# Optimization experiments

Hardware: AMD Instinct MI355X
Metric: run time of the kernel (lower is better)

## Reference

```python
import jax, jax.numpy as jnp
import numpy as np

HIDDEN = 4096
N_HEADS = 32
N_KV_HEADS = 8
HEAD_DIM = 128
ROPE_THETA = 1e6
RMS_EPS = 1e-6
SEQ = 2048


def setup_inputs() -> dict:
    key = jax.random.key(0)
    k1, k2, k3 = jax.random.split(key, 3)
    hidden_states = jax.random.normal(k1, (SEQ, HIDDEN), dtype=jnp.float32)
    # fused QKV weight: [hidden, (H + 2*Hkv) * head_dim]
    qkv_out = (N_HEADS + 2 * N_KV_HEADS) * HEAD_DIM
    w_qkv = jax.random.normal(k2, (HIDDEN, qkv_out), dtype=jnp.float32) * (HIDDEN ** -0.5)
    w_o = jax.random.normal(k3, (N_HEADS * HEAD_DIM, HIDDEN), dtype=jnp.float32) * ((N_HEADS * HEAD_DIM) ** -0.5)
    q_norm_w = jnp.ones((HEAD_DIM,), dtype=jnp.float32)
    k_norm_w = jnp.ones((HEAD_DIM,), dtype=jnp.float32)
    # NeoX-style rotary tables [T, head_dim/2]
    pos = jnp.arange(SEQ, dtype=jnp.float32)
    inv_freq = 1.0 / (ROPE_THETA ** (jnp.arange(0, HEAD_DIM, 2, dtype=jnp.float32) / HEAD_DIM))
    freqs = pos[:, None] * inv_freq[None, :]  # [T, d/2]
    cos = jnp.cos(freqs)
    sin = jnp.sin(freqs)
    return {"hidden_states": hidden_states, "cos": cos, "sin": sin,
            "w_qkv": w_qkv, "w_o": w_o, "q_norm_w": q_norm_w, "k_norm_w": k_norm_w}


def _rms_norm(x, w, eps=RMS_EPS):
    # per-head RMSNorm over last dim (head_dim)
    var = jnp.mean(jnp.square(x), axis=-1, keepdims=True)
    return x * jax.lax.rsqrt(var + eps) * w


def _rope(x, cos, sin):
    # NeoX rotate-half: x split into two halves of head_dim
    d2 = x.shape[-1] // 2
    x1, x2 = x[..., :d2], x[..., d2:]
    c = cos[:, None, :]  # [T,1,d/2] broadcast over heads
    s = sin[:, None, :]
    return jnp.concatenate([x1 * c - x2 * s, x2 * c + x1 * s], axis=-1)


def reference(hidden_states, cos, sin, w_qkv, w_o, q_norm_w, k_norm_w):
    T = hidden_states.shape[0]
    H, Hkv, D = N_HEADS, N_KV_HEADS, HEAD_DIM
    G = H // Hkv  # GQA group size
    scale = D ** -0.5

    qkv = hidden_states @ w_qkv  # [T, (H+2Hkv)*D]
    q, k, v = jnp.split(qkv, [H * D, (H + Hkv) * D], axis=1)
    q = q.reshape(T, H, D)
    k = k.reshape(T, Hkv, D)
    v = v.reshape(T, Hkv, D)

    q = _rms_norm(q, q_norm_w)
    k = _rms_norm(k, k_norm_w)
    q = _rope(q, cos, sin)
    k = _rope(k, cos, sin)

    # GQA: group query heads onto shared KV heads
    qg = q.reshape(T, Hkv, G, D)
    scores = jnp.einsum('qhgd,khd->hgqk', qg, k) * scale  # [Hkv,G,T,T]
    causal = jnp.tril(jnp.ones((T, T), dtype=bool))
    scores = jnp.where(causal, scores, jnp.float32(-1e30))
    probs = jax.nn.softmax(scores, axis=-1)
    out = jnp.einsum('hgqk,khd->qhgd', probs, v).reshape(T, H * D)
    return out @ w_o  # [T, hidden]
```

## Files before the change

### kernel.cpp

```cpp
#include <hip/hip_runtime.h>
#include <stdint.h>

#define SEQ   2048
#define HID   4096
#define NQH   32
#define NKVH  8
#define HD    128
#define QKVN  6144

typedef uint16_t u16;
typedef __attribute__((ext_vector_type(8))) short bf16x8;
typedef __attribute__((ext_vector_type(4))) float f32x4;
typedef __attribute__((ext_vector_type(4))) unsigned int u32x4;

static __device__ __forceinline__ float bf2f(u16 h){
  union { float f; unsigned int u; } v; v.u = ((unsigned int)h) << 16; return v.f;
}
static __device__ __forceinline__ u16 f2bf(float f){
  unsigned int u = __float_as_uint(f);
  return (u16)((u + 0x7fffu + ((u >> 16) & 1u)) >> 16);
}
static __device__ __forceinline__ f32x4 mfma16(bf16x8 a, bf16x8 b, f32x4 c){
  return __builtin_amdgcn_mfma_f32_16x16x32_bf16(a, b, c, 0, 0, 0);
}
static __device__ __forceinline__ void gload16(const void* g, void* l){
  __builtin_amdgcn_global_load_lds((const __attribute__((address_space(1))) void*)g,
                                   (__attribute__((address_space(3))) void*)l, 16, 0, 0);
}

__global__ void k_cvt(const float* __restrict__ src, u16* __restrict__ dst, int n4){
  int i = blockIdx.x * blockDim.x + threadIdx.x;
  if (i >= n4) return;
  float4 v = ((const float4*)src)[i];
  uint2 o;
  o.x = (unsigned)f2bf(v.x) | ((unsigned)f2bf(v.y) << 16);
  o.y = (unsigned)f2bf(v.z) | ((unsigned)f2bf(v.w) << 16);
  ((uint2*)dst)[i] = o;
}

__global__ void k_addf(const float* __restrict__ a, float* __restrict__ o, int n4){
  int i = blockIdx.x * blockDim.x + threadIdx.x;
  if (i >= n4) return;
  float4 x = ((const float4*)o)[i];
  float4 y = ((const float4*)a)[i];
  x.x += y.x; x.y += y.y; x.z += y.z; x.w += y.w;
  ((float4*)o)[i] = x;
}

__global__ void k_transpose_cvt(const float* __restrict__ src, u16* __restrict__ dst, int K, int N){
  __shared__ float t[32][33];
  int n0 = blockIdx.x * 32, k0 = blockIdx.y * 32;
  int tx = threadIdx.x, ty = threadIdx.y;
#pragma unroll
  for (int i = 0; i < 32; i += 8)
    t[ty + i][tx] = src[(size_t)(k0 + ty + i) * N + n0 + tx];
  __syncthreads();
#pragma unroll
  for (int i = 0; i < 32; i += 8)
    dst[(size_t)(n0 + ty + i) * K + k0 + tx] = f2bf(t[tx][ty + i]);
}

template<int OUTBF, int SPLITK, int XBC, int NBY>
__global__ __launch_bounds__(512) void k_gemm(const u16* __restrict__ A, const u16* __restrict__ Bt,
                                              void* __restrict__ Cv0, void* __restrict__ Cv1,
                                              int M, int N, int K){
  __shared__ __align__(16) u16 Asm[2][256][64];
  __shared__ __align__(16) u16 Bsm[2][256][64];
  const int tid = threadIdx.x, lane = tid & 63, wid = tid >> 6;
  const int wm = wid >> 2, wn = wid & 3;
  const int l16 = lane & 15, lhi = lane >> 4;
  const int rx = l16 & 7;
  const int bid = blockIdx.x;
  const int xcd = bid & 7, j = bid >> 3;
  const int bcol_i = xcd * XBC + j % XBC;
  const int rest = j / XBC;
  const int brow_i = rest % NBY;
  const int kz = (SPLITK > 1) ? (rest / NBY) : 0;
  const size_t brow = (size_t)brow_i * 256, bcol = (size_t)bcol_i * 256;
  const int kbeg = kz * (K / SPLITK);
  void* Cv = (kz == 0) ? Cv0 : Cv1;

  const f32x4 vz = {0.f, 0.f, 0.f, 0.f};
  f32x4 acc[8][4];
#pragma unroll
  for (int m = 0; m < 8; m++)
#pragma unroll
    for (int n = 0; n < 4; n++) acc[m][n] = vz;

  const int srow = lane >> 3;
  const int sg   = (lane & 7) ^ srow;
  const u16* Ags = A  + (brow + wid*8 + srow) * (size_t)K + sg*8 + kbeg;
  const u16* Bgs = Bt + (bcol + wid*8 + srow) * (size_t)K + sg*8 + kbeg;
  const int NT = (K / SPLITK) >> 6;

#pragma unroll
  for (int j2 = 0; j2 < 4; j2++) gload16(Ags + (size_t)j2*64*K, &Asm[0][wid*8 + j2*64][0]);
#pragma unroll
  for (int j2 = 0; j2 < 4; j2++) gload16(Bgs + (size_t)j2*64*K, &Bsm[0][wid*8 + j2*64][0]);
  asm volatile("s_waitcnt vmcnt(0)" ::: "memory");
  __builtin_amdgcn_sched_barrier(0);
  __builtin_amdgcn_s_barrier();

  for (int t = 0; t < NT; ++t){
    const int cur = t & 1, nxt = cur ^ 1;
    const size_t ko = (size_t)(t + 1) * 64;
    const bool st = (t + 1 < NT);
    bf16x8 a[8], b0, b1, b2, b3;
#pragma unroll
    for (int mi = 0; mi < 8; ++mi)
      a[mi] = *(const bf16x8*)&Asm[cur][wm*128 + mi*16 + l16][(lhi ^ rx) << 3];
    b0 = *(const bf16x8*)&Bsm[cur][wn*64 +  0 + l16][(lhi ^ rx) << 3];
    b1 = *(const bf16x8*)&Bsm[cur][wn*64 + 16 + l16][(lhi ^ rx) << 3];
    if (st){
      gload16(Ags + ko,                  &Asm[nxt][wid*8      ][0]);
      gload16(Ags + (size_t)64*K + ko,   &Asm[nxt][wid*8 +  64][0]);
      gload16(Bgs + ko,                  &Bsm[nxt][wid*8      ][0]);
      gload16(Bgs + (size_t)64*K + ko,   &Bsm[nxt][wid*8 +  64][0]);
    }
    __builtin_amdgcn_s_barrier();
    asm volatile("s_waitcnt lgkmcnt(0)" ::: "memory");
    __builtin_amdgcn_sched_barrier(0);
    __builtin_amdgcn_s_setprio(1);
#pragma unroll
    for (int mi = 0; mi < 8; ++mi){
      acc[mi][0] = mfma16(a[mi], b0, acc[mi][0]);
      acc[mi][1] = mfma16(a[mi], b1, acc[mi][1]);
    }
    __builtin_amdgcn_s_setprio(0);
    __builtin_amdgcn_s_barrier();
    b2 = *(const bf16x8*)&Bsm[cur][wn*64 + 32 + l16][(lhi ^ rx) << 3];
    b3 = *(const bf16x8*)&Bsm[cur][wn*64 + 48 + l16][(lhi ^ rx) << 3];
    if (st){
      gload16(Ags + (size_t)128*K + ko,  &Asm[nxt][wid*8 + 128][0]);
      gload16(Ags + (size_t)192*K + ko,  &Asm[nxt][wid*8 + 192][0]);
      gload16(Bgs + (size_t)128*K + ko,  &Bsm[nxt][wid*8 + 128][0]);
      gload16(Bgs + (size_t)192*K + ko,  &Bsm[nxt][wid*8 + 192][0]);
    }
    __builtin_amdgcn_s_barrier();
    asm volatile("s_waitcnt lgkmcnt(0)" ::: "memory");
    __builtin_amdgcn_sched_barrier(0);
    __builtin_amdgcn_s_setprio(1);
#pragma unroll
    for (int mi = 0; mi < 8; ++mi){
      acc[mi][2] = mfma16(a[mi], b2, acc[mi][2]);
      acc[mi][3] = mfma16(a[mi], b3, acc[mi][3]);
    }
    __builtin_amdgcn_s_setprio(0);
    __builtin_amdgcn_s_barrier();
#pragma unroll
    for (int mi = 0; mi < 8; ++mi)
      a[mi] = *(const bf16x8*)&Asm[cur][wm*128 + mi*16 + l16][((4 + lhi) ^ rx) << 3];
    b0 = *(const bf16x8*)&Bsm[cur][wn*64 +  0 + l16][((4 + lhi) ^ rx) << 3];
    b1 = *(const bf16x8*)&Bsm[cur][wn*64 + 16 + l16][((4 + lhi) ^ rx) << 3];
    __builtin_amdgcn_s_barrier();
    asm volatile("s_waitcnt lgkmcnt(0)" ::: "memory");
    __builtin_amdgcn_sched_barrier(0);
    __builtin_amdgcn_s_setprio(1);
#pragma unroll
    for (int mi = 0; mi < 8; ++mi){
      acc[mi][0] = mfma16(a[mi], b0, acc[mi][0]);
      acc[mi][1] = mfma16(a[mi], b1, acc[mi][1]);
    }
    __builtin_amdgcn_s_setprio(0);
    __builtin_amdgcn_s_barrier();
    b2 = *(const bf16x8*)&Bsm[cur][wn*64 + 32 + l16][((4 + lhi) ^ rx) << 3];
    b3 = *(const bf16x8*)&Bsm[cur][wn*64 + 48 + l16][((4 + lhi) ^ rx) << 3];
    __builtin_amdgcn_s_barrier();
    asm volatile("s_waitcnt lgkmcnt(0)" ::: "memory");
    __builtin_amdgcn_sched_barrier(0);
    __builtin_amdgcn_s_setprio(1);
#pragma unroll
    for (int mi = 0; mi < 8; ++mi){
      acc[mi][2] = mfma16(a[mi], b2, acc[mi][2]);
      acc[mi][3] = mfma16(a[mi], b3, acc[mi][3]);
    }
    __builtin_amdgcn_s_setprio(0);
    if (st){
      asm volatile("s_waitcnt vmcnt(0)" ::: "memory");
      __builtin_amdgcn_sched_barrier(0);
    }
    __builtin_amdgcn_s_barrier();
  }

#pragma unroll
  for (int mi = 0; mi < 8; mi++)
#pragma unroll
    for (int ni = 0; ni < 4; ni++)
#pragma unroll
      for (int i = 0; i < 4; i++){
        size_t row = brow + wm*128 + mi*16 + lhi*4 + i;
        size_t col = bcol + wn*64 + ni*16 + l16;
        if (OUTBF) ((u16*)Cv)[row * (size_t)N + col] = f2bf(acc[mi][ni][i]);
        else       ((float*)Cv)[row * (size_t)N + col] = acc[mi][ni][i];
      }
}

__global__ __launch_bounds__(256) void k_rmsrope(const u16* __restrict__ qkv, const float* __restrict__ cosp,
                                                 const float* __restrict__ sinp, const float* __restrict__ qw,
                                                 const float* __restrict__ kw, u16* __restrict__ Qr,
                                                 u16* __restrict__ Kr){
  int t = blockIdx.x;
  int lane = threadIdx.x & 63, w = threadIdx.x >> 6;
  int hh = blockIdx.y * 4 + w;
  bool isq = hh < NQH;
  int hl = isq ? hh : hh - NQH;
  const u16* src = qkv + (size_t)t * QKVN + (isq ? hl * HD : NQH * HD + hl * HD);
  unsigned u = *(const unsigned*)(src + 2 * lane);
  float x0 = bf2f((u16)(u & 0xffffu)), x1 = bf2f((u16)(u >> 16));
  float ss = x0 * x0 + x1 * x1;
#pragma unroll
  for (int m = 1; m < 64; m <<= 1) ss += __shfl_xor(ss, m);
  float rs = rsqrtf(ss * (1.f / HD) + 1e-6f);
  const float* wp = isq ? qw : kw;
  float w0 = wp[2 * lane], w1 = wp[2 * lane + 1];
  float xn0 = x0 * rs * w0, xn1 = x1 * rs * w1;
  float p0 = __shfl_xor(xn0, 32), p1 = __shfl_xor(xn1, 32);
  int j0 = (2 * lane) & 63;
  float c0 = cosp[t * 64 + j0], c1 = cosp[t * 64 + j0 + 1];
  float s0 = sinp[t * 64 + j0], s1 = sinp[t * 64 + j0 + 1];
  float o0, o1;
  if (lane < 32){ o0 = xn0 * c0 - p0 * s0; o1 = xn1 * c1 - p1 * s1; }
  else          { o0 = xn0 * c0 + p0 * s0; o1 = xn1 * c1 + p1 * s1; }
  if (isq){ o0 *= 0.08838834764831845f; o1 *= 0.08838834764831845f; }
  u16* dst = isq ? (Qr + ((size_t)hl * SEQ + t) * HD) : (Kr + ((size_t)hl * SEQ + t) * HD);
  *(unsigned*)(dst + 2 * lane) = (unsigned)f2bf(o0) | ((unsigned)f2bf(o1) << 16);
}

__global__ void k_vt(const u16* __restrict__ qkv, u16* __restrict__ VT){
  __shared__ u16 t[32][33];
  int t0 = blockIdx.x * 32, d0 = blockIdx.y * 32, hv = blockIdx.z;
  int tx = threadIdx.x, ty = threadIdx.y;
#pragma unroll
  for (int i = 0; i < 32; i += 8)
    t[ty + i][tx] = qkv[(size_t)(t0 + ty + i) * QKVN + (NQH + NKVH) * HD + hv * HD + d0 + tx];
  __syncthreads();
#pragma unroll
  for (int i = 0; i < 32; i += 8)
    VT[((size_t)hv * HD + d0 + ty + i) * SEQ + t0 + tx] = t[tx][ty + i];
}

__global__ __launch_bounds__(512) void k_attn(const u16* __restrict__ Q, const u16* __restrict__ Kg,
                                              const u16* __restrict__ VTg, u16* __restrict__ AO){
  __shared__ __align__(16) u16 Ksm[2][128][128];
  __shared__ __align__(16) u16 Vsm[128][128];
  __shared__ __align__(16) u16 Psm[8][16][136];
  int tid = threadIdx.x, lane = tid & 63, wid = tid >> 6;
  int l16 = lane & 15, lhi = lane >> 4;
  int bid = blockIdx.x;
  int kvg = bid & 7, rr = bid >> 3;
  int J = 15 - (rr >> 2);
  int hq = kvg * 4 + (rr & 3);
  int qb = J * 128;
  const u16* Kh = Kg  + (size_t)kvg * SEQ * HD;
  const u16* Vh = VTg + (size_t)kvg * HD * SEQ;
  const u16* Qh = Q   + (size_t)hq * SEQ * HD;

  bf16x8 qf[4];
#pragma unroll
  for (int ks = 0; ks < 4; ks++)
    qf[ks] = *(const bf16x8*)(Qh + (size_t)(qb + wid*16 + l16) * HD + ks*32 + lhi*8);

  const f32x4 vz = {0.f, 0.f, 0.f, 0.f};
  f32x4 o[8];
  float mrow[4], lrow[4];
#pragma unroll
  for (int n = 0; n < 8; n++) o[n] = vz;
#pragma unroll
  for (int i = 0; i < 4; i++){ mrow[i] = -1e30f; lrow[i] = 0.f; }

  int rsub = lane >> 4, g = lane & 15;
  const u16 *Ks0, *Ks1, *Ks2, *Ks3, *Vs0, *Vs1, *Vs2, *Vs3;
  {
    int r0 = wid*16 + 0*4 + rsub, r1 = wid*16 + 1*4 + rsub;
    int r2 = wid*16 + 2*4 + rsub, r3 = wid*16 + 3*4 + rsub;
    Ks0 = Kh + (size_t)r0 * HD + ((g ^ (r0 & 7)) << 3);
    Ks1 = Kh + (size_t)r1 * HD + ((g ^ (r1 & 7)) << 3);
    Ks2 = Kh + (size_t)r2 * HD + ((g ^ (r2 & 7)) << 3);
    Ks3 = Kh + (size_t)r3 * HD + ((g ^ (r3 & 7)) << 3);
    Vs0 = Vh + (size_t)r0 * SEQ + ((g ^ (r0 & 7)) << 3);
    Vs1 = Vh + (size_t)r1 * SEQ + ((g ^ (r1 & 7)) << 3);
    Vs2 = Vh + (size_t)r2 * SEQ + ((g ^ (r2 & 7)) << 3);
    Vs3 = Vh + (size_t)r3 * SEQ + ((g ^ (r3 & 7)) << 3);
  }

  gload16(Ks0, &Ksm[0][wid*16 +  0][0]);
  gload16(Ks1, &Ksm[0][wid*16 +  4][0]);
  gload16(Ks2, &Ksm[0][wid*16 +  8][0]);
  gload16(Ks3, &Ksm[0][wid*16 + 12][0]);
  asm volatile("s_waitcnt vmcnt(0)" ::: "memory");
  __builtin_amdgcn_sched_barrier(0);
  __builtin_amdgcn_s_barrier();

  int ntr = J + 1;
  int wrow0 = qb + wid*16;
  for (int t = 0; t < ntr; t++){
    int cur = t & 1, nxt = cur ^ 1;
    int kt0 = t << 7;
    bool pf = (t + 1 < ntr);
    gload16(Vs0 + kt0, &Vsm[wid*16 +  0][0]);
    gload16(Vs1 + kt0, &Vsm[wid*16 +  4][0]);
    gload16(Vs2 + kt0, &Vsm[wid*16 +  8][0]);
    gload16(Vs3 + kt0, &Vsm[wid*16 + 12][0]);
    if (pf){
      size_t ko = (size_t)(kt0 + 128) * HD;
      gload16(Ks0 + ko, &Ksm[nxt][wid*16 +  0][0]);
      gload16(Ks1 + ko, &Ksm[nxt][wid*16 +  4][0]);
      gload16(Ks2 + ko, &Ksm[nxt][wid*16 +  8][0]);
      gload16(Ks3 + ko, &Ksm[nxt][wid*16 + 12][0]);
    }
    f32x4 s[8];
#pragma unroll
    for (int n = 0; n < 8; n++) s[n] = vz;
    const u16* kbase = &Ksm[cur][0][0];
    __builtin_amdgcn_s_setprio(1);
#pragma unroll
    for (int n = 0; n < 8; n++){
      int row = n*16 + l16, rxk = row & 7;
#pragma unroll
      for (int ks = 0; ks < 4; ks++){
        bf16x8 kf = *(const bf16x8*)(kbase + row*128 + (((ks*4 + lhi) ^ rxk) << 3));
        s[n] = mfma16(qf[ks], kf, s[n]);
      }
    }
    __builtin_amdgcn_s_setprio(0);
    if (kt0 + 127 > wrow0){
#pragma unroll
      for (int n = 0; n < 8; n++)
#pragma unroll
        for (int i = 0; i < 4; i++)
          if (kt0 + n*16 + l16 > wrow0 + lhi*4 + i) s[n][i] = -1e30f;
    }
#pragma unroll
    for (int i = 0; i < 4; i++){
      float tm = fmaxf(fmaxf(fmaxf(s[0][i], s[1][i]), fmaxf(s[2][i], s[3][i])),
                       fmaxf(fmaxf(s[4][i], s[5][i]), fmaxf(s[6][i], s[7][i])));
      tm = fmaxf(tm, __shfl_xor(tm, 1));
      tm = fmaxf(tm, __shfl_xor(tm, 2));
      tm = fmaxf(tm, __shfl_xor(tm, 4));
      tm = fmaxf(tm, __shfl_xor(tm, 8));
      float nm = fmaxf(mrow[i], tm);
      float sc = __expf(mrow[i] - nm);
      mrow[i] = nm;
      float rsum = 0.f;
#pragma unroll
      for (int n = 0; n < 8; n++){
        float p = __expf(s[n][i] - nm);
        s[n][i] = p;
        rsum += p;
      }
      rsum += __shfl_xor(rsum, 1);
      rsum += __shfl_xor(rsum, 2);
      rsum += __shfl_xor(rsum, 4);
      rsum += __shfl_xor(rsum, 8);
      lrow[i] = lrow[i] * sc + rsum;
#pragma unroll
      for (int n = 0; n < 8; n++) o[n][i] *= sc;
    }
#pragma unroll
    for (int n = 0; n < 8; n++)
#pragma unroll
      for (int i = 0; i < 4; i++)
        Psm[wid][lhi*4 + i][n*16 + l16] = f2bf(s[n][i]);
    if (pf) asm volatile("s_waitcnt vmcnt(4)" ::: "memory");
    else    asm volatile("s_waitcnt vmcnt(0)" ::: "memory");
    __builtin_amdgcn_sched_barrier(0);
    __builtin_amdgcn_s_barrier();
    __builtin_amdgcn_sched_barrier(0);
    __builtin_amdgcn_s_setprio(1);
#pragma unroll
    for (int ksv = 0; ksv < 4; ksv++){
      bf16x8 pa = *(const bf16x8*)&Psm[wid][l16][ksv*32 + lhi*8];
#pragma unroll
      for (int n = 0; n < 8; n++){
        int row = n*16 + l16;
        bf16x8 vb = *(const bf16x8*)(&Vsm[0][0] + row*128 + (((ksv*4 + lhi) ^ (row & 7)) << 3));
        o[n] = mfma16(pa, vb, o[n]);
      }
    }
    __builtin_amdgcn_s_setprio(0);
    asm volatile("s_waitcnt vmcnt(0)" ::: "memory");
    __builtin_amdgcn_sched_barrier(0);
    __builtin_amdgcn_s_barrier();
  }
  float inv[4];
#pragma unroll
  for (int i = 0; i < 4; i++) inv[i] = 1.f / lrow[i];
#pragma unroll
  for (int n = 0; n < 8; n++)
#pragma unroll
    for (int i = 0; i < 4; i++){
      int trow = wrow0 + lhi*4 + i;
      AO[(size_t)trow * HID + hq * HD + n*16 + l16] = f2bf(o[n][i] * inv[i]);
    }
}

extern "C" void kernel_launch(void* const* d_in, const int* in_sizes, int n_in,
                              void* d_out, int out_size, void* d_ws, size_t ws_size,
                              hipStream_t stream){
  const float* hs   = (const float*)d_in[0];
  const float* cosp = (const float*)d_in[1];
  const float* sinp = (const float*)d_in[2];
  const float* wqkv = (const float*)d_in[3];
  const float* wo   = (const float*)d_in[4];
  const float* qw   = (const float*)d_in[5];
  const float* kw   = (const float*)d_in[6];
  float* out = (float*)d_out;
  char* ws = (char*)d_ws;
  u16* XB    = (u16*)(ws + 0);
  u16* WQKVT = (u16*)(ws + 16777216);
  u16* WOT   = (u16*)(ws + 0);
  float* SCR = (float*)(ws + 33554432);
  u16* QKV   = (u16*)(ws + 67108864);
  u16* QR    = (u16*)(ws + 92274688);
  u16* KR    = (u16*)(ws + 109051904);
  u16* VTB   = (u16*)(ws + 113246208);
  u16* AOB   = (u16*)(ws + 117440512);

  k_cvt<<<(SEQ * HID / 4 + 255) / 256, 256, 0, stream>>>(hs, XB, SEQ * HID / 4);
  k_transpose_cvt<<<dim3(QKVN / 32, HID / 32), dim3(32, 8), 0, stream>>>(wqkv, WQKVT, HID, QKVN);
  k_gemm<1, 1, 3, 8><<<192, 512, 0, stream>>>(XB, WQKVT, QKV, nullptr, SEQ, QKVN, HID);
  k_transpose_cvt<<<dim3(HID / 32, HID / 32), dim3(32, 8), 0, stream>>>(wo, WOT, HID, HID);
  k_rmsrope<<<dim3(SEQ, 10), 256, 0, stream>>>(QKV, cosp, sinp, qw, kw, QR, KR);
  k_vt<<<dim3(SEQ / 32, HD / 32, NKVH), dim3(32, 8), 0, stream>>>(QKV, VTB);
  k_attn<<<512, 512, 0, stream>>>(QR, KR, VTB, AOB);
  k_gemm<0, 2, 2, 8><<<256, 512, 0, stream>>>(AOB, WOT, out, SCR, SEQ, HID, HID);
  k_addf<<<SEQ * HID / 4 / 256, 256, 0, stream>>>(SCR, out, SEQ * HID / 4);
}
```

Before: 358.3 us.

## Restructure GEMM main loop into half-tile staged pipeline with split LDS buffers

Splits the LDS tiles into half-tile buffers and unrolls the K loop by two. Loads are staged per half-tile (A for the next tile, B two tiles ahead) between four quadrant MFMA phases. Each quadrant loads A fragments for both K halves at once and reuses them across B pairs. The aim is to hide more global-load latency behind compute and issue larger MFMA bursts between barriers, at the cost of more registers and more complex vmcnt bookkeeping. It also assumes an even tile count.

```diff
diff --git a/kernel.cpp b/kernel.cpp
--- a/kernel.cpp
+++ b/kernel.cpp
@@ -64,16 +64,16 @@
 __global__ __launch_bounds__(512) void k_gemm(const u16* __restrict__ A, const u16* __restrict__ Bt,
                                               void* __restrict__ Cv0, void* __restrict__ Cv1,
                                               int M, int N, int K){
-  __shared__ __align__(16) u16 Asm[2][256][64];
-  __shared__ __align__(16) u16 Bsm[2][256][64];
+  __shared__ __align__(16) u16 Asm[2][2][128][64];
+  __shared__ __align__(16) u16 Bsm[2][2][128][64];
   const int tid = threadIdx.x, lane = tid & 63, wid = tid >> 6;
   const int wm = wid >> 2, wn = wid & 3;
   const int l16 = lane & 15, lhi = lane >> 4;
   const int rx = l16 & 7;
   const int bid = blockIdx.x;
-  const int xcd = bid & 7, j = bid >> 3;
-  const int bcol_i = xcd * XBC + j % XBC;
-  const int rest = j / XBC;
+  const int xcd = bid & 7, jj = bid >> 3;
+  const int bcol_i = xcd * XBC + jj % XBC;
+  const int rest = jj / XBC;
   const int brow_i = rest % NBY;
   const int kz = (SPLITK > 1) ? (rest / NBY) : 0;
   const size_t brow = (size_t)brow_i * 256, bcol = (size_t)bcol_i * 256;
@@ -92,95 +92,167 @@
   const u16* Ags = A  + (brow + wid*8 + srow) * (size_t)K + sg*8 + kbeg;
   const u16* Bgs = Bt + (bcol + wid*8 + srow) * (size_t)K + sg*8 + kbeg;
   const int NT = (K / SPLITK) >> 6;
-
-#pragma unroll
-  for (int j2 = 0; j2 < 4; j2++) gload16(Ags + (size_t)j2*64*K, &Asm[0][wid*8 + j2*64][0]);
-#pragma unroll
-  for (int j2 = 0; j2 < 4; j2++) gload16(Bgs + (size_t)j2*64*K, &Bsm[0][wid*8 + j2*64][0]);
-  asm volatile("s_waitcnt vmcnt(0)" ::: "memory");
+  const int NU = NT >> 1;
+
+#define FRA(buf, mi, kh) (*(const bf16x8*)&Asm[buf][wm][(mi)*16 + l16][(((kh)*4 + lhi) ^ rx) << 3])
+#define FRB(buf, ni, kh) (*(const bf16x8*)&Bsm[buf][wn >> 1][(wn & 1)*64 + (ni)*16 + l16][(((kh)*4 + lhi) ^ rx) << 3])
+#define STG_A(tile, half) do{ if ((tile) < NT){                                  \
+    const size_t ko_ = (size_t)((half)*128) * K + (size_t)(tile) * 64;           \
+    gload16(Ags + ko_,                &Asm[(tile)&1][half][wid*8][0]);           \
+    gload16(Ags + ko_ + (size_t)64*K, &Asm[(tile)&1][half][64 + wid*8][0]); } }while(0)
+#define STG_B(tile, half) do{ if ((tile) < NT){                                  \
+    const size_t ko_ = (size_t)((half)*128) * K + (size_t)(tile) * 64;           \
+    gload16(Bgs + ko_,                &Bsm[(tile)&1][half][wid*8][0]);           \
+    gload16(Bgs + ko_ + (size_t)64*K, &Bsm[(tile)&1][half][64 + wid*8][0]); } }while(0)
+
+  STG_B(0, 0); STG_B(0, 1); STG_A(0, 0); STG_A(0, 1); STG_B(1, 0); STG_B(1, 1);
+  asm volatile("s_waitcnt vmcnt(4)" ::: "memory");
   __builtin_amdgcn_sched_barrier(0);
   __builtin_amdgcn_s_barrier();
 
-  for (int t = 0; t < NT; ++t){
-    const int cur = t & 1, nxt = cur ^ 1;
-    const size_t ko = (size_t)(t + 1) * 64;
-    const bool st = (t + 1 < NT);
-    bf16x8 a[8], b0, b1, b2, b3;
-#pragma unroll
-    for (int mi = 0; mi < 8; ++mi)
-      a[mi] = *(const bf16x8*)&Asm[cur][wm*128 + mi*16 + l16][(lhi ^ rx) << 3];
-    b0 = *(const bf16x8*)&Bsm[cur][wn*64 +  0 + l16][(lhi ^ rx) << 3];
-    b1 = *(const bf16x8*)&Bsm[cur][wn*64 + 16 + l16][(lhi ^ rx) << 3];
-    if (st){
-      gload16(Ags + ko,                  &Asm[nxt][wid*8      ][0]);
-      gload16(Ags + (size_t)64*K + ko,   &Asm[nxt][wid*8 +  64][0]);
-      gload16(Bgs + ko,                  &Bsm[nxt][wid*8      ][0]);
-      gload16(Bgs + (size_t)64*K + ko,   &Bsm[nxt][wid*8 +  64][0]);
-    }
-    __builtin_amdgcn_s_barrier();
-    asm volatile("s_waitcnt lgkmcnt(0)" ::: "memory");
-    __builtin_amdgcn_sched_barrier(0);
-    __builtin_amdgcn_s_setprio(1);
-#pragma unroll
-    for (int mi = 0; mi < 8; ++mi){
-      acc[mi][0] = mfma16(a[mi], b0, acc[mi][0]);
-      acc[mi][1] = mfma16(a[mi], b1, acc[mi][1]);
-    }
-    __builtin_amdgcn_s_setprio(0);
-    __builtin_amdgcn_s_barrier();
-    b2 = *(const bf16x8*)&Bsm[cur][wn*64 + 32 + l16][(lhi ^ rx) << 3];
-    b3 = *(const bf16x8*)&Bsm[cur][wn*64 + 48 + l16][(lhi ^ rx) << 3];
-    if (st){
-      gload16(Ags + (size_t)128*K + ko,  &Asm[nxt][wid*8 + 128][0]);
-      gload16(Ags + (size_t)192*K + ko,  &Asm[nxt][wid*8 + 192][0]);
-      gload16(Bgs + (size_t)128*K + ko,  &Bsm[nxt][wid*8 + 128][0]);
-      gload16(Bgs + (size_t)192*K + ko,  &Bsm[nxt][wid*8 + 192][0]);
-    }
-    __builtin_amdgcn_s_barrier();
-    asm volatile("s_waitcnt lgkmcnt(0)" ::: "memory");
-    __builtin_amdgcn_sched_barrier(0);
-    __builtin_amdgcn_s_setprio(1);
-#pragma unroll
-    for (int mi = 0; mi < 8; ++mi){
-      acc[mi][2] = mfma16(a[mi], b2, acc[mi][2]);
-      acc[mi][3] = mfma16(a[mi], b3, acc[mi][3]);
-    }
-    __builtin_amdgcn_s_setprio(0);
-    __builtin_amdgcn_s_barrier();
-#pragma unroll
-    for (int mi = 0; mi < 8; ++mi)
-      a[mi] = *(const bf16x8*)&Asm[cur][wm*128 + mi*16 + l16][((4 + lhi) ^ rx) << 3];
-    b0 = *(const bf16x8*)&Bsm[cur][wn*64 +  0 + l16][((4 + lhi) ^ rx) << 3];
-    b1 = *(const bf16x8*)&Bsm[cur][wn*64 + 16 + l16][((4 + lhi) ^ rx) << 3];
-    __builtin_amdgcn_s_barrier();
-    asm volatile("s_waitcnt lgkmcnt(0)" ::: "memory");
-    __builtin_amdgcn_sched_barrier(0);
-    __builtin_amdgcn_s_setprio(1);
-#pragma unroll
-    for (int mi = 0; mi < 8; ++mi){
-      acc[mi][0] = mfma16(a[mi], b0, acc[mi][0]);
-      acc[mi][1] = mfma16(a[mi], b1, acc[mi][1]);
-    }
-    __builtin_amdgcn_s_setprio(0);
-    __builtin_amdgcn_s_barrier();
-    b2 = *(const bf16x8*)&Bsm[cur][wn*64 + 32 + l16][((4 + lhi) ^ rx) << 3];
-    b3 = *(const bf16x8*)&Bsm[cur][wn*64 + 48 + l16][((4 + lhi) ^ rx) << 3];
-    __builtin_amdgcn_s_barrier();
-    asm volatile("s_waitcnt lgkmcnt(0)" ::: "memory");
-    __builtin_amdgcn_sched_barrier(0);
-    __builtin_amdgcn_s_setprio(1);
-#pragma unroll
-    for (int mi = 0; mi < 8; ++mi){
-      acc[mi][2] = mfma16(a[mi], b2, acc[mi][2]);
-      acc[mi][3] = mfma16(a[mi], b3, acc[mi][3]);
-    }
-    __builtin_amdgcn_s_setprio(0);
-    if (st){
-      asm volatile("s_waitcnt vmcnt(0)" ::: "memory");
-      __builtin_amdgcn_sched_barrier(0);
-    }
+  bf16x8 fA[4][2], fB01[2][2], fB23[2][2];
+  for (int u = 0; u < NU; ++u){
+    const int t = 2 * u;
+#pragma unroll
+    for (int mi = 0; mi < 4; ++mi){ fA[mi][0] = FRA(0, mi, 0); fA[mi][1] = FRA(0, mi, 1); }
+#pragma unroll
+    for (int ni = 0; ni < 2; ++ni){ fB01[ni][0] = FRB(0, ni, 0); fB01[ni][1] = FRB(0, ni, 1); }
+    STG_A(t + 1, 0);
+    asm volatile("s_waitcnt lgkmcnt(8)" ::: "memory");
+    __builtin_amdgcn_s_barrier();
+    asm volatile("s_waitcnt lgkmcnt(0)" ::: "memory");
+    __builtin_amdgcn_sched_barrier(0);
+    __builtin_amdgcn_s_setprio(1);
+#pragma unroll
+    for (int kh = 0; kh < 2; ++kh)
+#pragma unroll
+      for (int mi = 0; mi < 4; ++mi)
+#pragma unroll
+        for (int ni = 0; ni < 2; ++ni)
+          acc[mi][ni] = mfma16(fA[mi][kh], fB01[ni][kh], acc[mi][ni]);
+    __builtin_amdgcn_s_setprio(0);
+    __builtin_amdgcn_s_barrier();
+#pragma unroll
+    for (int ni = 0; ni < 2; ++ni){ fB23[ni][0] = FRB(0, 2 + ni, 0); fB23[ni][1] = FRB(0, 2 + ni, 1); }
+    STG_A(t + 1, 1);
+    __builtin_amdgcn_s_barrier();
+    asm volatile("s_waitcnt lgkmcnt(0)" ::: "memory");
+    __builtin_amdgcn_sched_barrier(0);
+    __builtin_amdgcn_s_setprio(1);
+#pragma unroll
+    for (int kh = 0; kh < 2; ++kh)
+#pragma unroll
+      for (int mi = 0; mi < 4; ++mi)
+#pragma unroll
+        for (int ni = 0; ni < 2; ++ni)
+          acc[mi][2 + ni] = mfma16(fA[mi][kh], fB23[ni][kh], acc[mi][2 + ni]);
+    __builtin_amdgcn_s_setprio(0);
+    __builtin_amdgcn_s_barrier();
+#pragma unroll
+    for (int mi = 0; mi < 4; ++mi){ fA[mi][0] = FRA(0, 4 + mi, 0); fA[mi][1] = FRA(0, 4 + mi, 1); }
+    STG_B(t + 2, 0);
+    __builtin_amdgcn_s_barrier();
+    asm volatile("s_waitcnt lgkmcnt(0)" ::: "memory");
+    __builtin_amdgcn_sched_barrier(0);
+    __builtin_amdgcn_s_setprio(1);
+#pragma unroll
+    for (int kh = 0; kh < 2; ++kh)
+#pragma unroll
+      for (int mi = 0; mi < 4; ++mi)
+#pragma unroll
+        for (int ni = 0; ni < 2; ++ni)
+          acc[4 + mi][ni] = mfma16(fA[mi][kh], fB01[ni][kh], acc[4 + mi][ni]);
+    __builtin_amdgcn_s_setprio(0);
+    __builtin_amdgcn_s_barrier();
+    STG_B(t + 2, 1);
+    __builtin_amdgcn_s_barrier();
+    asm volatile("s_waitcnt lgkmcnt(0)" ::: "memory");
+    __builtin_amdgcn_sched_barrier(0);
+    __builtin_amdgcn_s_setprio(1);
+#pragma unroll
+    for (int kh = 0; kh < 2; ++kh)
+#pragma unroll
+      for (int mi = 0; mi < 4; ++mi)
+#pragma unroll
+        for (int ni = 0; ni < 2; ++ni)
+          acc[4 + mi][2 + ni] = mfma16(fA[mi][kh], fB23[ni][kh], acc[4 + mi][2 + ni]);
+    __builtin_amdgcn_s_setprio(0);
+    if (u == NU - 1) asm volatile("s_waitcnt vmcnt(0)" ::: "memory");
+    else             asm volatile("s_waitcnt vmcnt(4)" ::: "memory");
+    __builtin_amdgcn_sched_barrier(0);
+    __builtin_amdgcn_s_barrier();
+#pragma unroll
+    for (int mi = 0; mi < 4; ++mi){ fA[mi][0] = FRA(1, mi, 0); fA[mi][1] = FRA(1, mi, 1); }
+#pragma unroll
+    for (int ni = 0; ni < 2; ++ni){ fB01[ni][0] = FRB(1, ni, 0); fB01[ni][1] = FRB(1, ni, 1); }
+    STG_A(t + 2, 0);
+    asm volatile("s_waitcnt lgkmcnt(8)" ::: "memory");
+    __builtin_amdgcn_s_barrier();
+    asm volatile("s_waitcnt lgkmcnt(0)" ::: "memory");
+    __builtin_amdgcn_sched_barrier(0);
+    __builtin_amdgcn_s_setprio(1);
+#pragma unroll
+    for (int kh = 0; kh < 2; ++kh)
+#pragma unroll
+      for (int mi = 0; mi < 4; ++mi)
+#pragma unroll
+        for (int ni = 0; ni < 2; ++ni)
+          acc[mi][ni] = mfma16(fA[mi][kh], fB01[ni][kh], acc[mi][ni]);
+    __builtin_amdgcn_s_setprio(0);
+    __builtin_amdgcn_s_barrier();
+#pragma unroll
+    for (int ni = 0; ni < 2; ++ni){ fB23[ni][0] = FRB(1, 2 + ni, 0); fB23[ni][1] = FRB(1, 2 + ni, 1); }
+    STG_A(t + 2, 1);
+    __builtin_amdgcn_s_barrier();
+    asm volatile("s_waitcnt lgkmcnt(0)" ::: "memory");
+    __builtin_amdgcn_sched_barrier(0);
+    __builtin_amdgcn_s_setprio(1);
+#pragma unroll
+    for (int kh = 0; kh < 2; ++kh)
+#pragma unroll
+      for (int mi = 0; mi < 4; ++mi)
+#pragma unroll
+        for (int ni = 0; ni < 2; ++ni)
+          acc[mi][2 + ni] = mfma16(fA[mi][kh], fB23[ni][kh], acc[mi][2 + ni]);
+    __builtin_amdgcn_s_setprio(0);
+    __builtin_amdgcn_s_barrier();
+#pragma unroll
+    for (int mi = 0; mi < 4; ++mi){ fA[mi][0] = FRA(1, 4 + mi, 0); fA[mi][1] = FRA(1, 4 + mi, 1); }
+    STG_B(t + 3, 0);
+    __builtin_amdgcn_s_barrier();
+    asm volatile("s_waitcnt lgkmcnt(0)" ::: "memory");
+    __builtin_amdgcn_sched_barrier(0);
+    __builtin_amdgcn_s_setprio(1);
+#pragma unroll
+    for (int kh = 0; kh < 2; ++kh)
+#pragma unroll
+      for (int mi = 0; mi < 4; ++mi)
+#pragma unroll
+        for (int ni = 0; ni < 2; ++ni)
+          acc[4 + mi][ni] = mfma16(fA[mi][kh], fB01[ni][kh], acc[4 + mi][ni]);
+    __builtin_amdgcn_s_setprio(0);
+    __builtin_amdgcn_s_barrier();
+    STG_B(t + 3, 1);
+    __builtin_amdgcn_s_barrier();
+    asm volatile("s_waitcnt lgkmcnt(0)" ::: "memory");
+    __builtin_amdgcn_sched_barrier(0);
+    __builtin_amdgcn_s_setprio(1);
+#pragma unroll
+    for (int kh = 0; kh < 2; ++kh)
+#pragma unroll
+      for (int mi = 0; mi < 4; ++mi)
+#pragma unroll
+        for (int ni = 0; ni < 2; ++ni)
+          acc[4 + mi][2 + ni] = mfma16(fA[mi][kh], fB23[ni][kh], acc[4 + mi][2 + ni]);
+    __builtin_amdgcn_s_setprio(0);
+    asm volatile("s_waitcnt vmcnt(4)" ::: "memory");
+    __builtin_amdgcn_sched_barrier(0);
     __builtin_amdgcn_s_barrier();
   }
+#undef FRA
+#undef FRB
+#undef STG_A
+#undef STG_B
 
 #pragma unroll
   for (int mi = 0; mi < 8; mi++)
```

Result: faster. 344.9 us (-3.7%).
